# Kernel optimization log

Measured on AMD Instinct MI355X. Metric: run time of the kernel, lower is better.

Reference implementation:

```python
import math
import jax, jax.numpy as jnp
import numpy as np

D_MODEL = 1024
N_HEADS = 16
D_K = D_MODEL // N_HEADS  # 64
D_C = 256
B, S = 2, 2048


def setup_inputs() -> dict:
    key = jax.random.key(0)
    ks = jax.random.split(key, 7)
    sd = lambda fan_in: 1.0 / math.sqrt(fan_in)
    # weights stored as [in, out] so forward is x @ W
    return {
        "x": jax.random.normal(ks[0], (B, S, D_MODEL), dtype=jnp.float32),
        "W_dq": jax.random.uniform(ks[1], (D_MODEL, D_C), minval=-sd(D_MODEL), maxval=sd(D_MODEL), dtype=jnp.float32),
        "W_uq": jax.random.uniform(ks[2], (D_C, N_HEADS * D_K), minval=-sd(D_C), maxval=sd(D_C), dtype=jnp.float32),
        "W_dkv": jax.random.uniform(ks[3], (D_MODEL, D_C), minval=-sd(D_MODEL), maxval=sd(D_MODEL), dtype=jnp.float32),
        "W_uk": jax.random.uniform(ks[4], (D_C, N_HEADS * D_K), minval=-sd(D_C), maxval=sd(D_C), dtype=jnp.float32),
        "W_uv": jax.random.uniform(ks[5], (D_C, N_HEADS * D_K), minval=-sd(D_C), maxval=sd(D_C), dtype=jnp.float32),
        "W_o": jax.random.uniform(ks[6], (N_HEADS * D_K, D_MODEL), minval=-sd(N_HEADS * D_K), maxval=sd(N_HEADS * D_K), dtype=jnp.float32),
    }


def reference(x, W_dq, W_uq, W_dkv, W_uk, W_uv, W_o):
    Bx, Sx, _ = x.shape
    c_q = x @ W_dq                                   # [B,S,d_c]
    Q = (c_q @ W_uq).reshape(Bx, Sx, N_HEADS, D_K)   # [B,S,H,dk]
    c_kv = x @ W_dkv                                 # [B,S,d_c]
    K = (c_kv @ W_uk).reshape(Bx, Sx, N_HEADS, D_K)
    V = (c_kv @ W_uv).reshape(Bx, Sx, N_HEADS, D_K)
    scores = jnp.einsum("bqhd,bkhd->bhqk", Q, K) / math.sqrt(D_K)
    causal = jnp.tril(jnp.ones((Sx, Sx), dtype=bool))
    scores = jnp.where(causal, scores, -jnp.inf)
    attn = jax.nn.softmax(scores, axis=-1)           # [B,H,S,S]
    out = jnp.einsum("bhqk,bkhd->bqhd", attn, V).reshape(Bx, Sx, N_HEADS * D_K)
    return out @ W_o
```

## Files before the change

### kernel.cpp

```cpp
#include <hip/hip_runtime.h>
#include <math.h>

#define AS3 __attribute__((address_space(3)))
#define AS1 __attribute__((address_space(1)))

typedef unsigned short u16;
typedef unsigned int u32;
typedef __bf16 bf16_t;
typedef bf16_t bf16x8 __attribute__((ext_vector_type(8)));
typedef float f32x4 __attribute__((ext_vector_type(4)));
typedef float f32x16 __attribute__((ext_vector_type(16)));
typedef unsigned short u16x4 __attribute__((ext_vector_type(4)));
typedef unsigned short u16x8 __attribute__((ext_vector_type(8)));
typedef unsigned int u32x4 __attribute__((ext_vector_type(4)));

#define NH 16
#define DK 64
#define DC 256
#define DM 1024
#define BB 2
#define SS 2048
#define TT (BB*SS)

__device__ __forceinline__ u16 f2bf(float f) {
    unsigned u = __builtin_bit_cast(unsigned, f);
    unsigned r = (u + 0x7FFFu + ((u >> 16) & 1u)) >> 16;
    return (u16)r;
}

__device__ __forceinline__ float bf2f(u16 h) {
    u32 u = ((u32)h) << 16;
    return __builtin_bit_cast(float, u);
}

__device__ __forceinline__ u32 cvtpk_bf16(float a, float b) {
    u32 d;
    asm("v_cvt_pk_bf16_f32 %0, %1, %2" : "=v"(d) : "v"(a), "v"(b));
    return d;
}

__device__ __forceinline__ bf16x8 lds_frag(const char* p) {
    return __builtin_bit_cast(bf16x8, *reinterpret_cast<const u16x8*>(p));
}

__global__ __launch_bounds__(256) void prep(const float* w0, const float* w1, const float* w2,
                                            const float* w3, const float* w4, const float* w5,
                                            u16* d0, u16* d1, u16* d2, u16* d3, u16* d4, u16* d5) {
    __shared__ float t[32][33];
    const int z = blockIdx.z;
    const float* src; u16* dst; int R, C, opitch;
    switch (z) {
        case 0:  src = w0; dst = d0; R = 1024; C = 256;  opitch = 1024; break;
        case 1:  src = w1; dst = d1; R = 1024; C = 256;  opitch = 1024; break;
        case 2:  src = w2; dst = d2; R = 256;  C = 1024; opitch = 256;  break;
        case 3:  src = w3; dst = d3; R = 256;  C = 1024; opitch = 256;  break;
        case 4:  src = w4; dst = d4; R = 256;  C = 1024; opitch = 256;  break;
        default: src = w5; dst = d5; R = 1024; C = 1024; opitch = 1024; break;
    }
    int c0 = blockIdx.x * 32, r0 = blockIdx.y * 32;
    if (c0 >= C || r0 >= R) return;
    int tx = threadIdx.x & 31, ty = threadIdx.x >> 5;
    #pragma unroll
    for (int p = 0; p < 4; ++p)
        t[ty + 8 * p][tx] = src[(r0 + ty + 8 * p) * C + c0 + tx];
    __syncthreads();
    #pragma unroll
    for (int p = 0; p < 4; ++p)
        dst[(c0 + ty + 8 * p) * opitch + r0 + tx] = f2bf(t[tx][ty + 8 * p]);
}

__global__ __launch_bounds__(256) void gemm_dqkv(const float* __restrict__ X,
                                                 const u16* __restrict__ Bt,
                                                 u16* __restrict__ Cc) {
    __shared__ u16 As[2][64 * 32];
    __shared__ u16 Bs[2][64 * 32];
    const int tid = threadIdx.x;
    const int lane = tid & 63;
    const int w = tid >> 6;
    const int wr = w >> 1, wc = w & 1;
    const int bm = blockIdx.x * 64, bn = blockIdx.y * 64;
    const int l15 = lane & 15, l4 = lane >> 4;
    const int arow = tid >> 2, akc = (tid & 3) * 8;

    f32x4 acc[2][2] = {};

    for (int k0 = 0; k0 < 1024; k0 += 64) {
        #pragma unroll
        for (int h = 0; h < 2; ++h) {
            const float* xp = X + (size_t)(bm + arow) * 1024 + k0 + h * 32 + akc;
            float4 v0 = *reinterpret_cast<const float4*>(xp);
            float4 v1 = *reinterpret_cast<const float4*>(xp + 4);
            u32x4 o;
            o.x = cvtpk_bf16(v0.x, v0.y);
            o.y = cvtpk_bf16(v0.z, v0.w);
            o.z = cvtpk_bf16(v1.x, v1.y);
            o.w = cvtpk_bf16(v1.z, v1.w);
            *reinterpret_cast<u32x4*>(&As[h][arow * 32 + akc]) = o;
        }
        #pragma unroll
        for (int h = 0; h < 2; ++h) {
            __builtin_amdgcn_global_load_lds(
                (const AS1 void*)(Bt + (size_t)(bn + arow) * 1024 + k0 + h * 32 + akc),
                (AS3 void*)((AS3 char*)(AS3 void*)&Bs[h][0] + w * 1024), 16, 0, 0);
        }
        __syncthreads();
        #pragma unroll
        for (int h = 0; h < 2; ++h) {
            bf16x8 a[2], b[2];
            #pragma unroll
            for (int m = 0; m < 2; ++m)
                a[m] = __builtin_bit_cast(bf16x8,
                    *reinterpret_cast<const u16x8*>(&As[h][(wr * 32 + m * 16 + l15) * 32 + l4 * 8]));
            #pragma unroll
            for (int n = 0; n < 2; ++n)
                b[n] = __builtin_bit_cast(bf16x8,
                    *reinterpret_cast<const u16x8*>(&Bs[h][(wc * 32 + n * 16 + l15) * 32 + l4 * 8]));
            #pragma unroll
            for (int m = 0; m < 2; ++m)
                #pragma unroll
                for (int n = 0; n < 2; ++n)
                    acc[m][n] = __builtin_amdgcn_mfma_f32_16x16x32_bf16(a[m], b[n], acc[m][n], 0, 0, 0);
        }
        __syncthreads();
    }
    #pragma unroll
    for (int m = 0; m < 2; ++m) {
        int row = bm + wr * 32 + m * 16 + l4 * 4;
        #pragma unroll
        for (int j = 0; j < 4; ++j)
            #pragma unroll
            for (int n = 0; n < 2; ++n) {
                int col = bn + wc * 32 + n * 16 + l15;
                Cc[(size_t)(row + j) * 512 + col] = f2bf(acc[m][n][j]);
            }
    }
}

__global__ __launch_bounds__(256) void gemm_out(const u16* __restrict__ A,
                                                const u16* __restrict__ Bt,
                                                float* __restrict__ C) {
    __shared__ u16 As[2][64 * 32];
    __shared__ u16 Bs[2][128 * 32];
    const int tid = threadIdx.x;
    const int lane = tid & 63;
    const int w = tid >> 6;
    const int wr = w >> 1, wc = w & 1;
    const int bm = blockIdx.x * 64, bn = blockIdx.y * 128;
    const int l15 = lane & 15, l4 = lane >> 4;

    f32x4 acc[2][4] = {};

    for (int k0 = 0; k0 < 1024; k0 += 64) {
        #pragma unroll
        for (int h = 0; h < 2; ++h) {
            {
                int db = tid * 16;
                int row = db >> 6;
                int kc = (db & 63) >> 1;
                __builtin_amdgcn_global_load_lds(
                    (const AS1 void*)(A + (size_t)(bm + row) * 1024 + k0 + h * 32 + kc),
                    (AS3 void*)((AS3 char*)(AS3 void*)&As[h][0] + w * 1024), 16, 0, 0);
            }
            #pragma unroll
            for (int i = 0; i < 2; ++i) {
                int db = i * 4096 + tid * 16;
                int row = db >> 6;
                int kc = (db & 63) >> 1;
                __builtin_amdgcn_global_load_lds(
                    (const AS1 void*)(Bt + (size_t)(bn + row) * 1024 + k0 + h * 32 + kc),
                    (AS3 void*)((AS3 char*)(AS3 void*)&Bs[h][0] + i * 4096 + w * 1024), 16, 0, 0);
            }
        }
        __syncthreads();
        #pragma unroll
        for (int h = 0; h < 2; ++h) {
            bf16x8 a[2], b[4];
            #pragma unroll
            for (int m = 0; m < 2; ++m)
                a[m] = __builtin_bit_cast(bf16x8,
                    *reinterpret_cast<const u16x8*>(&As[h][(wr * 32 + m * 16 + l15) * 32 + l4 * 8]));
            #pragma unroll
            for (int n = 0; n < 4; ++n)
                b[n] = __builtin_bit_cast(bf16x8,
                    *reinterpret_cast<const u16x8*>(&Bs[h][(wc * 64 + n * 16 + l15) * 32 + l4 * 8]));
            #pragma unroll
            for (int m = 0; m < 2; ++m)
                #pragma unroll
                for (int n = 0; n < 4; ++n)
                    acc[m][n] = __builtin_amdgcn_mfma_f32_16x16x32_bf16(a[m], b[n], acc[m][n], 0, 0, 0);
        }
        __syncthreads();
    }
    #pragma unroll
    for (int m = 0; m < 2; ++m) {
        int row = bm + wr * 32 + m * 16 + l4 * 4;
        #pragma unroll
        for (int j = 0; j < 4; ++j)
            #pragma unroll
            for (int n = 0; n < 4; ++n) {
                int col = bn + wc * 64 + n * 16 + l15;
                C[(size_t)(row + j) * 1024 + col] = acc[m][n][j];
            }
    }
}

template <int OUT_MODE>
__device__ __forceinline__ void gemm_body128(const u16* __restrict__ A, int lda,
                                             const u16* __restrict__ Bt, int ldb,
                                             void* __restrict__ C, int ldc, int K,
                                             int bm, int bn, u16* As, u16* Bs) {
    const int tid = threadIdx.x;
    const int lane = tid & 63;
    const int w = tid >> 6;
    const int wr = w >> 1, wc = w & 1;
    const int l15 = lane & 15, l4 = lane >> 4;

    f32x4 acc[4][4] = {};

    for (int k0 = 0; k0 < K; k0 += 32) {
        #pragma unroll
        for (int i = 0; i < 2; ++i) {
            int db = i * 4096 + tid * 16;
            int row = db >> 6;
            int kc = (db & 63) >> 1;
            __builtin_amdgcn_global_load_lds(
                (const AS1 void*)(A + (size_t)(bm + row) * lda + k0 + kc),
                (AS3 void*)((AS3 char*)(AS3 void*)As + i * 4096 + w * 1024), 16, 0, 0);
            __builtin_amdgcn_global_load_lds(
                (const AS1 void*)(Bt + (size_t)(bn + row) * ldb + k0 + kc),
                (AS3 void*)((AS3 char*)(AS3 void*)Bs + i * 4096 + w * 1024), 16, 0, 0);
        }
        __syncthreads();
        bf16x8 a[4], b[4];
        #pragma unroll
        for (int m = 0; m < 4; ++m)
            a[m] = __builtin_bit_cast(bf16x8,
                *reinterpret_cast<const u16x8*>(&As[(wr * 64 + m * 16 + l15) * 32 + l4 * 8]));
        #pragma unroll
        for (int n = 0; n < 4; ++n)
            b[n] = __builtin_bit_cast(bf16x8,
                *reinterpret_cast<const u16x8*>(&Bs[(wc * 64 + n * 16 + l15) * 32 + l4 * 8]));
        #pragma unroll
        for (int m = 0; m < 4; ++m)
            #pragma unroll
            for (int n = 0; n < 4; ++n)
                acc[m][n] = __builtin_amdgcn_mfma_f32_16x16x32_bf16(a[m], b[n], acc[m][n], 0, 0, 0);
        __syncthreads();
    }
    if (OUT_MODE == 2) {
        #pragma unroll
        for (int m = 0; m < 4; ++m) {
            int row = bm + wr * 64 + m * 16 + l4 * 4;
            int vrow_base = (row >> 11) << 10;
            int scol = row & 2047;
            #pragma unroll
            for (int n = 0; n < 4; ++n) {
                int col = bn + wc * 64 + n * 16 + l15;
                u16x4 ov;
                ov[0] = f2bf(acc[m][n][0]); ov[1] = f2bf(acc[m][n][1]);
                ov[2] = f2bf(acc[m][n][2]); ov[3] = f2bf(acc[m][n][3]);
                *reinterpret_cast<u16x4*>((u16*)C + (size_t)(vrow_base + col) * 2048 + scol) = ov;
            }
        }
    } else {
        #pragma unroll
        for (int m = 0; m < 4; ++m) {
            int row = bm + wr * 64 + m * 16 + l4 * 4;
            #pragma unroll
            for (int j = 0; j < 4; ++j)
                #pragma unroll
                for (int n = 0; n < 4; ++n) {
                    int col = bn + wc * 64 + n * 16 + l15;
                    ((u16*)C)[(size_t)(row + j) * ldc + col] = f2bf(acc[m][n][j]);
                }
        }
    }
}

__global__ __launch_bounds__(256) void gemm_qkv(const u16* __restrict__ c_qkv,
                                                const u16* __restrict__ Wuq_t,
                                                const u16* __restrict__ Wukv_t,
                                                u16* __restrict__ Qb, u16* __restrict__ Kb,
                                                u16* __restrict__ Vt) {
    __shared__ u16 As[128 * 32];
    __shared__ u16 Bs[128 * 32];
    const int by = blockIdx.y;
    const int bm = blockIdx.x * 128;
    if (by < 8) {
        gemm_body128<1>(c_qkv, 512, Wuq_t, 256, Qb, 1024, 256,
                        bm, by * 128, As, Bs);
    } else if (by < 16) {
        gemm_body128<1>(c_qkv + 256, 512, Wukv_t, 256, Kb, 1024, 256,
                        bm, (by - 8) * 128, As, Bs);
    } else {
        gemm_body128<2>(c_qkv + 256, 512, Wukv_t + 1024 * 256, 256, Vt, 0, 256,
                        bm, (by - 16) * 128, As, Bs);
    }
}

__global__ __launch_bounds__(256, 4) void attn_mfma6(const u16* __restrict__ Qb,
                                                     const u16* __restrict__ Kb,
                                                     const u16* __restrict__ VtG,
                                                     u16* __restrict__ O) {
    __shared__ char lds[32768];
    const int bid = blockIdx.x;
    const int g = bid >> 8, u = (bid >> 5) & 7;
    const int bq = (g == 0) ? (31 - u) : (g == 1) ? (16 + u) : (g == 2) ? (15 - u) : u;
    const int bh = bid & 31;
    const int b = bh >> 4, head = bh & 15;
    const int tid = threadIdx.x;
    const int w = tid >> 6;
    const int lane = tid & 63;
    const int l31 = lane & 31, hi = lane >> 5;
    const int r7 = l31 & 7;
    const int pair = w >> 1, sub = w & 1;
    const int q0 = bq * 64;
    const int qg = q0 + sub * 32 + l31;
    const int rounds = (bq >> 1) + 1;
    const float c2 = 0.125f * 1.44269504088896340736f;

    bf16x8 qf[4];
    {
        const u16* qp = Qb + (size_t)(b * SS + qg) * 1024 + head * 64 + hi * 8;
        #pragma unroll
        for (int kc = 0; kc < 4; ++kc)
            qf[kc] = __builtin_bit_cast(bf16x8, *reinterpret_cast<const u16x8*>(qp + kc * 16));
    }

    f32x16 acc0 = {}, acc1 = {};
    float lrow = 0.f;

#define STAGE2(r_) do { \
    _Pragma("unroll") \
    for (int p_ = 0; p_ < 2; ++p_) { \
        int kt_ = 2 * (r_) + p_; \
        if (kt_ <= bq) { \
            int k0_ = kt_ * 64; \
            char* base_ = lds + p_ * 16384; \
            _Pragma("unroll") \
            for (int c_ = 0; c_ < 2; ++c_) { \
                int i_ = tid + 256 * c_; int row_ = i_ >> 3; int sc_ = (i_ & 7) ^ (row_ & 7); \
                __builtin_amdgcn_global_load_lds( \
                    (const AS1 void*)(Kb + (size_t)(b * SS + k0_ + row_) * 1024 + head * 64 + sc_ * 8), \
                    (AS3 void*)((AS3 char*)(AS3 void*)base_ + c_ * 4096 + w * 1024), 16, 0, 0); \
                __builtin_amdgcn_global_load_lds( \
                    (const AS1 void*)(VtG + (size_t)(bh * 64 + row_) * 2048 + k0_ + sc_ * 8), \
                    (AS3 void*)((AS3 char*)(AS3 void*)base_ + 8192 + c_ * 4096 + w * 1024), 16, 0, 0); \
            } \
        } \
    } } while (0)

    for (int r = 0; r < rounds; ++r) {
        STAGE2(r);
        __syncthreads();
        const int kt = 2 * r + pair;
        if (kt <= bq) {
            const char* Kb_ = lds + pair * 16384;
            const char* Vb_ = Kb_ + 8192;
            const int k0 = kt * 64;
            f32x16 s0 = {}, s1 = {};
            __builtin_amdgcn_s_setprio(1);
            #pragma unroll
            for (int kc = 0; kc < 4; ++kc) {
                bf16x8 kf0 = lds_frag(Kb_ + (l31) * 128 + ((2 * kc + hi) ^ r7) * 16);
                bf16x8 kf1 = lds_frag(Kb_ + (32 + l31) * 128 + ((2 * kc + hi) ^ r7) * 16);
                s0 = __builtin_amdgcn_mfma_f32_32x32x16_bf16(kf0, qf[kc], s0, 0, 0, 0);
                s1 = __builtin_amdgcn_mfma_f32_32x32x16_bf16(kf1, qf[kc], s1, 0, 0, 0);
            }
            __builtin_amdgcn_s_setprio(0);
            if (kt == bq) {
                const int lim = qg - k0 - hi * 4;
                #pragma unroll
                for (int r2 = 0; r2 < 16; ++r2) {
                    const int ko = (r2 & 3) + 8 * (r2 >> 2);
                    s0[r2] = (ko > lim) ? -3.0e38f : s0[r2];
                    s1[r2] = (ko + 32 > lim) ? -3.0e38f : s1[r2];
                }
            }
            #pragma unroll
            for (int r2 = 0; r2 < 16; ++r2) {
                s0[r2] = exp2f(s0[r2] * c2);
                s1[r2] = exp2f(s1[r2] * c2);
            }
            float c8[8];
            #pragma unroll
            for (int i = 0; i < 8; ++i)
                c8[i] = (s0[2 * i] + s0[2 * i + 1]) + (s1[2 * i] + s1[2 * i + 1]);
            float rsum = ((c8[0] + c8[1]) + (c8[2] + c8[3])) + ((c8[4] + c8[5]) + (c8[6] + c8[7]));
            rsum += __shfl_xor(rsum, 32);
            lrow += rsum;
            u32 cg0[4][2], cg1[4][2];
            #pragma unroll
            for (int gg = 0; gg < 4; ++gg) {
                #pragma unroll
                for (int w2 = 0; w2 < 2; ++w2) {
                    cg0[gg][w2] = cvtpk_bf16(s0[4 * gg + 2 * w2], s0[4 * gg + 2 * w2 + 1]);
                    cg1[gg][w2] = cvtpk_bf16(s1[4 * gg + 2 * w2], s1[4 * gg + 2 * w2 + 1]);
                }
            }
            bf16x8 pa[4];
            #pragma unroll
            for (int ks = 0; ks < 4; ++ks) {
                const int g0 = (2 * ks) & 3, g1 = g0 + 1;
                u32 a0, a1, b0, b1;
                if (ks < 2) { a0 = cg0[g0][0]; a1 = cg0[g0][1]; b0 = cg0[g1][0]; b1 = cg0[g1][1]; }
                else        { a0 = cg1[g0][0]; a1 = cg1[g0][1]; b0 = cg1[g1][0]; b1 = cg1[g1][1]; }
                u32 pa0 = (u32)__shfl_xor((int)a0, 32);
                u32 pa1 = (u32)__shfl_xor((int)a1, 32);
                u32 pb0 = (u32)__shfl_xor((int)b0, 32);
                u32 pb1 = (u32)__shfl_xor((int)b1, 32);
                u32x4 f;
                f.x = hi ? pb0 : a0;
                f.y = hi ? pb1 : a1;
                f.z = hi ? b0 : pa0;
                f.w = hi ? b1 : pa1;
                pa[ks] = __builtin_bit_cast(bf16x8, f);
            }
            __builtin_amdgcn_s_setprio(1);
            #pragma unroll
            for (int ks = 0; ks < 4; ++ks) {
                bf16x8 vf0 = lds_frag(Vb_ + (l31) * 128 + ((2 * ks + hi) ^ r7) * 16);
                bf16x8 vf1 = lds_frag(Vb_ + (32 + l31) * 128 + ((2 * ks + hi) ^ r7) * 16);
                acc0 = __builtin_amdgcn_mfma_f32_32x32x16_bf16(vf0, pa[ks], acc0, 0, 0, 0);
                acc1 = __builtin_amdgcn_mfma_f32_32x32x16_bf16(vf1, pa[ks], acc1, 0, 0, 0);
            }
            __builtin_amdgcn_s_setprio(0);
        }
        __syncthreads();
    }
#undef STAGE2

    u16* partb = (u16*)lds;
    float* mls = (float*)(lds + 18432);
    #pragma unroll
    for (int r2 = 0; r2 < 16; r2 += 2) {
        const int d0 = (r2 & 3) + 8 * (r2 >> 2) + 4 * hi;
        *reinterpret_cast<u32*>(&partb[(w * 32 + l31) * 72 + d0]) =
            cvtpk_bf16(acc0[r2], acc0[r2 + 1]);
        *reinterpret_cast<u32*>(&partb[(w * 32 + l31) * 72 + d0 + 32]) =
            cvtpk_bf16(acc1[r2], acc1[r2 + 1]);
    }
    if (hi == 0 && lane < 32) mls[w * 32 + l31] = lrow;
    __syncthreads();

    {
        const int q = tid >> 2, ds0 = (tid & 3) * 16;
        const int s_ = q >> 5, qq = q & 31;
        const int wa_ = s_, wb_ = 2 + s_;
        float lt = mls[wa_ * 32 + qq] + mls[wb_ * 32 + qq];
        float inv = 1.0f / lt;
        u16x8 pa0 = *reinterpret_cast<const u16x8*>(&partb[(wa_ * 32 + qq) * 72 + ds0]);
        u16x8 pa1 = *reinterpret_cast<const u16x8*>(&partb[(wa_ * 32 + qq) * 72 + ds0 + 8]);
        u16x8 pb0 = *reinterpret_cast<const u16x8*>(&partb[(wb_ * 32 + qq) * 72 + ds0]);
        u16x8 pb1 = *reinterpret_cast<const u16x8*>(&partb[(wb_ * 32 + qq) * 72 + ds0 + 8]);
        u16x8 ov0, ov1;
        #pragma unroll
        for (int i = 0; i < 8; ++i) {
            float v0 = bf2f(pa0[i]) + bf2f(pb0[i]);
            float v1 = bf2f(pa1[i]) + bf2f(pb1[i]);
            ov0[i] = f2bf(v0 * inv);
            ov1[i] = f2bf(v1 * inv);
        }
        u16* op = O + (size_t)(b * SS + q0 + q) * 1024 + head * 64 + ds0;
        *reinterpret_cast<u16x8*>(op) = ov0;
        *reinterpret_cast<u16x8*>(op + 8) = ov1;
    }
}


extern "C" void kernel_launch(void* const* d_in, const int* in_sizes, int n_in,
                              void* d_out, int out_size, void* d_ws, size_t ws_size,
                              hipStream_t stream) {
    const float* x     = (const float*)d_in[0];
    const float* W_dq  = (const float*)d_in[1];
    const float* W_uq  = (const float*)d_in[2];
    const float* W_dkv = (const float*)d_in[3];
    const float* W_uk  = (const float*)d_in[4];
    const float* W_uv  = (const float*)d_in[5];
    const float* W_o   = (const float*)d_in[6];
    float* out = (float*)d_out;

    char* ws = (char*)d_ws;
    u16* c_qkv   = (u16*)(ws + (8u << 20));
    u16* Qb      = (u16*)(ws + (12u << 20));
    u16* Kb      = (u16*)(ws + (20u << 20));
    u16* Vt      = (u16*)(ws + (36u << 20));
    u16* attno   = (u16*)(ws + (44u << 20));
    u16* Wdqkv_t = (u16*)(ws + (52u << 20));
    u16* Wuq_t   = (u16*)(ws + (53u << 20));
    u16* Wukv_t  = (u16*)(ws + (53u << 20) + (512u << 10));
    u16* Wo_t    = (u16*)(ws + (55u << 20));

    dim3 blk(256);
    prep<<<dim3(32, 32, 6), blk, 0, stream>>>(W_dq, W_dkv, W_uq, W_uk, W_uv, W_o,
        Wdqkv_t, Wdqkv_t + 256 * 1024, Wuq_t, Wukv_t, Wukv_t + 1024 * 256, Wo_t);
    gemm_dqkv<<<dim3(64, 8), blk, 0, stream>>>(x, Wdqkv_t, c_qkv);
    gemm_qkv<<<dim3(32, 24), blk, 0, stream>>>(c_qkv, Wuq_t, Wukv_t, Qb, Kb, Vt);
    attn_mfma6<<<dim3(1024), blk, 0, stream>>>(Qb, Kb, Vt, attno);
    gemm_out<<<dim3(64, 8), blk, 0, stream>>>(attno, Wo_t, out);
}
```

Before: 94.14 us.

## Use 512-thread attention blocks covering 128 queries to share K/V tiles

The attention kernel now runs 512 threads per block, each block handling 128 query rows with 8 waves: 4 query sub-tiles times 2 key-tile pairs. Each staged K/V tile in LDS is therefore reused by twice as many queries, halving global K/V traffic per query and halving the grid. The final split-K merge now has pair-1 waves write partials and pair-0 waves combine them directly from registers. The risks are fewer blocks, which means coarser causal load balance, and waves idling on diagonal tiles that are fully masked for their query sub-tile.

```diff
diff --git a/kernel.cpp b/kernel.cpp
--- a/kernel.cpp
+++ b/kernel.cpp
@@ -12,6 +12,7 @@
 typedef float f32x16 __attribute__((ext_vector_type(16)));
 typedef unsigned short u16x4 __attribute__((ext_vector_type(4)));
 typedef unsigned short u16x8 __attribute__((ext_vector_type(8)));
+typedef unsigned int u32x2 __attribute__((ext_vector_type(2)));
 typedef unsigned int u32x4 __attribute__((ext_vector_type(4)));
 
 #define NH 16
@@ -298,14 +299,14 @@
     }
 }
 
-__global__ __launch_bounds__(256, 4) void attn_mfma6(const u16* __restrict__ Qb,
+__global__ __launch_bounds__(512, 4) void attn_mfma8(const u16* __restrict__ Qb,
                                                      const u16* __restrict__ Kb,
                                                      const u16* __restrict__ VtG,
                                                      u16* __restrict__ O) {
     __shared__ char lds[32768];
     const int bid = blockIdx.x;
     const int g = bid >> 8, u = (bid >> 5) & 7;
-    const int bq = (g == 0) ? (31 - u) : (g == 1) ? (16 + u) : (g == 2) ? (15 - u) : u;
+    const int bq = g ? u : (15 - u);
     const int bh = bid & 31;
     const int b = bh >> 4, head = bh & 15;
     const int tid = threadIdx.x;
@@ -313,10 +314,13 @@
     const int lane = tid & 63;
     const int l31 = lane & 31, hi = lane >> 5;
     const int r7 = l31 & 7;
-    const int pair = w >> 1, sub = w & 1;
-    const int q0 = bq * 64;
-    const int qg = q0 + sub * 32 + l31;
-    const int rounds = (bq >> 1) + 1;
+    const int pair = w & 1;
+    const int qs = w >> 1;
+    const int q0 = bq * 128;
+    const int qbase = q0 + qs * 32;
+    const int qg = qbase + l31;
+    const int qtop = qbase + 31;
+    const int rounds = bq + 1;
     const float c2 = 0.125f * 1.44269504088896340736f;
 
     bf16x8 qf[4];
@@ -330,31 +334,24 @@
     f32x16 acc0 = {}, acc1 = {};
     float lrow = 0.f;
 
-#define STAGE2(r_) do { \
-    _Pragma("unroll") \
-    for (int p_ = 0; p_ < 2; ++p_) { \
-        int kt_ = 2 * (r_) + p_; \
-        if (kt_ <= bq) { \
-            int k0_ = kt_ * 64; \
-            char* base_ = lds + p_ * 16384; \
-            _Pragma("unroll") \
-            for (int c_ = 0; c_ < 2; ++c_) { \
-                int i_ = tid + 256 * c_; int row_ = i_ >> 3; int sc_ = (i_ & 7) ^ (row_ & 7); \
-                __builtin_amdgcn_global_load_lds( \
-                    (const AS1 void*)(Kb + (size_t)(b * SS + k0_ + row_) * 1024 + head * 64 + sc_ * 8), \
-                    (AS3 void*)((AS3 char*)(AS3 void*)base_ + c_ * 4096 + w * 1024), 16, 0, 0); \
-                __builtin_amdgcn_global_load_lds( \
-                    (const AS1 void*)(VtG + (size_t)(bh * 64 + row_) * 2048 + k0_ + sc_ * 8), \
-                    (AS3 void*)((AS3 char*)(AS3 void*)base_ + 8192 + c_ * 4096 + w * 1024), 16, 0, 0); \
-            } \
-        } \
-    } } while (0)
+    const int srow = tid >> 3;
+    const int ssc = (tid & 7) ^ (srow & 7);
 
     for (int r = 0; r < rounds; ++r) {
-        STAGE2(r);
+        #pragma unroll
+        for (int p_ = 0; p_ < 2; ++p_) {
+            const int k0_ = (2 * r + p_) * 64;
+            char* base_ = lds + p_ * 16384;
+            __builtin_amdgcn_global_load_lds(
+                (const AS1 void*)(Kb + (size_t)(b * SS + k0_ + srow) * 1024 + head * 64 + ssc * 8),
+                (AS3 void*)((AS3 char*)(AS3 void*)base_ + w * 1024), 16, 0, 0);
+            __builtin_amdgcn_global_load_lds(
+                (const AS1 void*)(VtG + (size_t)(bh * 64 + srow) * 2048 + k0_ + ssc * 8),
+                (AS3 void*)((AS3 char*)(AS3 void*)base_ + 8192 + w * 1024), 16, 0, 0);
+        }
         __syncthreads();
         const int kt = 2 * r + pair;
-        if (kt <= bq) {
+        if (kt * 64 <= qtop) {
             const char* Kb_ = lds + pair * 16384;
             const char* Vb_ = Kb_ + 8192;
             const int k0 = kt * 64;
@@ -368,7 +365,7 @@
                 s1 = __builtin_amdgcn_mfma_f32_32x32x16_bf16(kf1, qf[kc], s1, 0, 0, 0);
             }
             __builtin_amdgcn_s_setprio(0);
-            if (kt == bq) {
+            if (k0 + 63 > qbase) {
                 const int lim = qg - k0 - hi * 4;
                 #pragma unroll
                 for (int r2 = 0; r2 < 16; ++r2) {
@@ -428,42 +425,45 @@
         }
         __syncthreads();
     }
-#undef STAGE2
 
     u16* partb = (u16*)lds;
-    float* mls = (float*)(lds + 18432);
-    #pragma unroll
-    for (int r2 = 0; r2 < 16; r2 += 2) {
-        const int d0 = (r2 & 3) + 8 * (r2 >> 2) + 4 * hi;
-        *reinterpret_cast<u32*>(&partb[(w * 32 + l31) * 72 + d0]) =
-            cvtpk_bf16(acc0[r2], acc0[r2 + 1]);
-        *reinterpret_cast<u32*>(&partb[(w * 32 + l31) * 72 + d0 + 32]) =
-            cvtpk_bf16(acc1[r2], acc1[r2 + 1]);
-    }
-    if (hi == 0 && lane < 32) mls[w * 32 + l31] = lrow;
+    float* l1 = (float*)(lds + 18432);
+    if (pair == 1) {
+        #pragma unroll
+        for (int r2 = 0; r2 < 16; r2 += 2) {
+            const int d0 = (r2 & 3) + 8 * (r2 >> 2) + 4 * hi;
+            *reinterpret_cast<u32*>(&partb[(qs * 32 + l31) * 72 + d0]) =
+                cvtpk_bf16(acc0[r2], acc0[r2 + 1]);
+            *reinterpret_cast<u32*>(&partb[(qs * 32 + l31) * 72 + d0 + 32]) =
+                cvtpk_bf16(acc1[r2], acc1[r2 + 1]);
+        }
+        if (hi == 0) l1[qs * 32 + l31] = lrow;
+    }
     __syncthreads();
-
-    {
-        const int q = tid >> 2, ds0 = (tid & 3) * 16;
-        const int s_ = q >> 5, qq = q & 31;
-        const int wa_ = s_, wb_ = 2 + s_;
-        float lt = mls[wa_ * 32 + qq] + mls[wb_ * 32 + qq];
-        float inv = 1.0f / lt;
-        u16x8 pa0 = *reinterpret_cast<const u16x8*>(&partb[(wa_ * 32 + qq) * 72 + ds0]);
-        u16x8 pa1 = *reinterpret_cast<const u16x8*>(&partb[(wa_ * 32 + qq) * 72 + ds0 + 8]);
-        u16x8 pb0 = *reinterpret_cast<const u16x8*>(&partb[(wb_ * 32 + qq) * 72 + ds0]);
-        u16x8 pb1 = *reinterpret_cast<const u16x8*>(&partb[(wb_ * 32 + qq) * 72 + ds0 + 8]);
-        u16x8 ov0, ov1;
-        #pragma unroll
-        for (int i = 0; i < 8; ++i) {
-            float v0 = bf2f(pa0[i]) + bf2f(pb0[i]);
-            float v1 = bf2f(pa1[i]) + bf2f(pb1[i]);
-            ov0[i] = f2bf(v0 * inv);
-            ov1[i] = f2bf(v1 * inv);
-        }
-        u16* op = O + (size_t)(b * SS + q0 + q) * 1024 + head * 64 + ds0;
-        *reinterpret_cast<u16x8*>(op) = ov0;
-        *reinterpret_cast<u16x8*>(op + 8) = ov1;
+    if (pair == 0) {
+        const float inv = 1.0f / (lrow + l1[qs * 32 + l31]);
+        u16* orow = O + (size_t)(b * SS + qbase + l31) * 1024 + head * 64 + 4 * hi;
+        #pragma unroll
+        for (int k = 0; k < 4; ++k) {
+            u16x4 p0 = *reinterpret_cast<const u16x4*>(&partb[(qs * 32 + l31) * 72 + 8 * k + 4 * hi]);
+            u16x4 p1 = *reinterpret_cast<const u16x4*>(&partb[(qs * 32 + l31) * 72 + 8 * k + 4 * hi + 32]);
+            float m0 = (acc0[4 * k + 0] + bf2f(p0[0])) * inv;
+            float m1 = (acc0[4 * k + 1] + bf2f(p0[1])) * inv;
+            float m2 = (acc0[4 * k + 2] + bf2f(p0[2])) * inv;
+            float m3 = (acc0[4 * k + 3] + bf2f(p0[3])) * inv;
+            u32x2 o0;
+            o0.x = cvtpk_bf16(m0, m1);
+            o0.y = cvtpk_bf16(m2, m3);
+            *reinterpret_cast<u32x2*>(orow + 8 * k) = o0;
+            float n0 = (acc1[4 * k + 0] + bf2f(p1[0])) * inv;
+            float n1 = (acc1[4 * k + 1] + bf2f(p1[1])) * inv;
+            float n2 = (acc1[4 * k + 2] + bf2f(p1[2])) * inv;
+            float n3 = (acc1[4 * k + 3] + bf2f(p1[3])) * inv;
+            u32x2 o1;
+            o1.x = cvtpk_bf16(n0, n1);
+            o1.y = cvtpk_bf16(n2, n3);
+            *reinterpret_cast<u32x2*>(orow + 32 + 8 * k) = o1;
+        }
     }
 }
 
@@ -496,6 +496,6 @@
         Wdqkv_t, Wdqkv_t + 256 * 1024, Wuq_t, Wukv_t, Wukv_t + 1024 * 256, Wo_t);
     gemm_dqkv<<<dim3(64, 8), blk, 0, stream>>>(x, Wdqkv_t, c_qkv);
     gemm_qkv<<<dim3(32, 24), blk, 0, stream>>>(c_qkv, Wuq_t, Wukv_t, Qb, Kb, Vt);
-    attn_mfma6<<<dim3(1024), blk, 0, stream>>>(Qb, Kb, Vt, attno);
+    attn_mfma8<<<dim3(512), dim3(512), 0, stream>>>(Qb, Kb, Vt, attno);
     gemm_out<<<dim3(64, 8), blk, 0, stream>>>(attno, Wo_t, out);
 }
```

Measured after the change: 99.28 us. +5.5%, slower.
